# Kernel optimization log

Hardware: AMD Instinct MI355X
Metric: run time of the kernel (lower is better)

The kernel has to match this reference:

```python
import jax, jax.numpy as jnp
import numpy as np


def setup_inputs() -> dict:
    key = jax.random.key(0)
    k1, k2, k3, k4 = jax.random.split(key, 4)
    T = 64            # decoder_batch_len (target steps)
    B = 32            # batch_size
    V = 50257         # decoder vocab size
    L = 400           # encoder (source) length
    rows = T * B
    vocab_ds = jax.random.uniform(k1, (rows, V), dtype=jnp.float32)
    attns = jax.random.uniform(k2, (rows, L), dtype=jnp.float32)
    p_gens = jax.random.uniform(k3, (rows, 1), dtype=jnp.float32)
    sources = jax.random.randint(k4, (L, B), 0, V, dtype=jnp.int64)
    return {
        "vocab_ds": vocab_ds,
        "attns": attns,
        "p_gens": p_gens,
        "sources": sources,
        "decoder_batch_len": T,
    }


def reference(vocab_ds, attns, p_gens, sources, decoder_batch_len):
    # vocab_ds: (T*B, V), attns: (T*B, L), p_gens: (T*B, 1), sources: (L, B)
    rows, V = vocab_ds.shape
    vocab_dists = p_gens * vocab_ds                      # gated generation dist
    attn_dists = (1.0 - p_gens) * attns                  # gated copy dist
    # sources.T tiled over decoder steps -> per-row vocab ids, shape (T*B, L)
    sources_rep = jnp.tile(sources.T, (decoder_batch_len, 1))
    row_idx = jnp.arange(rows)[:, None]                  # (T*B, 1) broadcasts over L
    # torch scatter_ (overwrite semantics) of copy probs into vocab slots
    attn_dists_projected = jnp.zeros((rows, V), dtype=vocab_ds.dtype).at[
        row_idx, sources_rep
    ].set(attn_dists, mode="drop")
    final_dists = attn_dists_projected + vocab_dists
    return final_dists
```

## Files before the change

### kernel.cpp

```cpp
#include <hip/hip_runtime.h>

typedef float f32x4 __attribute__((ext_vector_type(4)));

#define LMAX 1024

__global__ __launch_bounds__(256) void mask_kernel(
    const int* __restrict__ sources, int* __restrict__ vlast, int L, int B)
{
    const int b = blockIdx.x;
    __shared__ int s_col[LMAX];
    const bool use_lds = (L <= LMAX);
    if (use_lds) {
        for (int l = threadIdx.x; l < L; l += blockDim.x)
            s_col[l] = sources[(size_t)l * B + b];
    }
    __syncthreads();
    for (int l = threadIdx.x; l < L; l += blockDim.x) {
        const int v = use_lds ? s_col[l] : sources[(size_t)l * B + b];
        int keep = v;
        if (use_lds) {
            for (int l2 = l + 1; l2 < L; ++l2)
                if (s_col[l2] == v) { keep = -1; break; }
        } else {
            for (int l2 = l + 1; l2 < L; ++l2)
                if (sources[(size_t)l2 * B + b] == v) { keep = -1; break; }
        }
        vlast[(size_t)l * B + b] = keep;
    }
}

__global__ __launch_bounds__(256) void scale_kernel(
    const float* __restrict__ vd, const float* __restrict__ pgs,
    float* __restrict__ out, int V)
{
    const int row = blockIdx.x;
    const int tid = threadIdx.x;
    const size_t base = (size_t)row * (size_t)V;
    const float pg = pgs[row];

    const int mis  = (int)(base & 3);
    const int pre  = mis ? (4 - mis) : 0;
    const int preN = pre < V ? pre : V;
    for (int j = tid; j < preN; j += 256)
        __builtin_nontemporal_store(pg * vd[base + j], &out[base + j]);

    const int nvec = (V - preN) >> 2;
    const f32x4* __restrict__ v4 = (const f32x4*)(vd + base + preN);
    f32x4* __restrict__ o4       = (f32x4*)(out + base + preN);

    int i = tid;
    for (; i + 3 * 256 < nvec; i += 4 * 256) {
        f32x4 a = v4[i];
        f32x4 b = v4[i + 256];
        f32x4 c = v4[i + 512];
        f32x4 d = v4[i + 768];
        a *= pg; b *= pg; c *= pg; d *= pg;
        __builtin_nontemporal_store(a, &o4[i]);
        __builtin_nontemporal_store(b, &o4[i + 256]);
        __builtin_nontemporal_store(c, &o4[i + 512]);
        __builtin_nontemporal_store(d, &o4[i + 768]);
    }
    for (; i < nvec; i += 256) {
        f32x4 a = v4[i];
        a *= pg;
        __builtin_nontemporal_store(a, &o4[i]);
    }
    for (int j = preN + (nvec << 2) + tid; j < V; j += 256)
        __builtin_nontemporal_store(pg * vd[base + j], &out[base + j]);
}

__global__ __launch_bounds__(128) void scatter_kernel(
    const float* __restrict__ vd, const float* __restrict__ attns,
    const float* __restrict__ pgs, const int* __restrict__ vlast,
    float* __restrict__ out, int V, int L, int B)
{
    const int row = blockIdx.x;
    const int b = row % B;
    const float pg = pgs[row];
    const float gate = 1.0f - pg;
    const size_t base = (size_t)row * (size_t)V;
    for (int l = threadIdx.x; l < L; l += 128) {
        const int v = vlast[(size_t)l * B + b];
        if (v >= 0 && v < V)
            out[base + v] = fmaf(pg, vd[base + v],
                                 gate * attns[(size_t)row * L + l]);
    }
}

__global__ __launch_bounds__(256) void fused_fallback_kernel(
    const float* __restrict__ vocab_ds, const float* __restrict__ attns,
    const float* __restrict__ p_gens, const int* __restrict__ sources,
    float* __restrict__ out, int V, int L, int B)
{
    const int row = blockIdx.x;
    const int tid = threadIdx.x;
    const size_t base = (size_t)row * (size_t)V;
    const float pg = p_gens[row];

    const int mis  = (int)(base & 3);
    const int pre  = mis ? (4 - mis) : 0;
    const int preN = pre < V ? pre : V;
    for (int j = tid; j < preN; j += blockDim.x)
        out[base + j] = pg * vocab_ds[base + j];
    const int nvec = (V - preN) >> 2;
    const f32x4* __restrict__ v4 = (const f32x4*)(vocab_ds + base + preN);
    f32x4* __restrict__ o4       = (f32x4*)(out + base + preN);
    for (int i = tid; i < nvec; i += blockDim.x) {
        f32x4 x = v4[i];
        x *= pg;
        o4[i] = x;
    }
    for (int j = preN + (nvec << 2) + tid; j < V; j += blockDim.x)
        out[base + j] = pg * vocab_ds[base + j];

    __shared__ int s_src[512];
    const int b = row % B;
    const bool use_lds = (L <= 512);
    if (use_lds) {
        for (int l = tid; l < L; l += blockDim.x)
            s_src[l] = sources[(size_t)l * B + b];
    }
    __syncthreads();
    const float gate = 1.0f - pg;
    for (int l = tid; l < L; l += blockDim.x) {
        const int v = use_lds ? s_src[l] : sources[(size_t)l * B + b];
        if (v < 0 || v >= V) continue;
        bool last = true;
        for (int l2 = l + 1; l2 < L; ++l2) {
            const int v2 = use_lds ? s_src[l2] : sources[(size_t)l2 * B + b];
            if (v2 == v) { last = false; break; }
        }
        if (last) {
            const float a = gate * attns[(size_t)row * L + l];
            out[base + v] = pg * vocab_ds[base + v] + a;
        }
    }
}

extern "C" void kernel_launch(void* const* d_in, const int* in_sizes, int n_in,
                              void* d_out, int out_size, void* d_ws, size_t ws_size,
                              hipStream_t stream) {
    const float* vocab_ds = (const float*)d_in[0];
    const float* attns    = (const float*)d_in[1];
    const float* p_gens   = (const float*)d_in[2];
    const int*   sources  = (const int*)d_in[3];
    const int rows = in_sizes[2];
    const int V    = in_sizes[0] / rows;
    const int L    = in_sizes[1] / rows;
    const int B    = in_sizes[3] / L;
    float* out = (float*)d_out;

    const size_t mask_bytes = (size_t)L * (size_t)B * sizeof(int);
    if (ws_size >= mask_bytes) {
        int* vlast = (int*)d_ws;
        mask_kernel<<<B, 256, 0, stream>>>(sources, vlast, L, B);
        scale_kernel<<<rows, 256, 0, stream>>>(vocab_ds, p_gens, out, V);
        scatter_kernel<<<rows, 128, 0, stream>>>(vocab_ds, attns, p_gens,
                                                 vlast, out, V, L, B);
    } else {
        fused_fallback_kernel<<<rows, 256, 0, stream>>>(
            vocab_ds, attns, p_gens, sources, out, V, L, B);
    }
}
```

Baseline: 248.6 us.

## Split each row of scale kernel across multiple blocks and use regular stores

The scale kernel now launches several blocks per row, each handling a contiguous chunk of the row's float4 vectors, instead of one block per row. This raises the number of in-flight blocks so memory bandwidth is easier to saturate. Nontemporal stores and the 4-way unrolled loop are replaced by plain stores in a simple loop, so written data may now stay in cache for the scatter kernel to read. The scatter kernel's block size goes from 128 to 256 threads.

```diff
diff --git a/kernel.cpp b/kernel.cpp
--- a/kernel.cpp
+++ b/kernel.cpp
@@ -31,45 +31,39 @@
 
 __global__ __launch_bounds__(256) void scale_kernel(
     const float* __restrict__ vd, const float* __restrict__ pgs,
-    float* __restrict__ out, int V)
+    float* __restrict__ out, int V, int CPR)
 {
-    const int row = blockIdx.x;
-    const int tid = threadIdx.x;
+    const int bid   = blockIdx.x;
+    const int row   = bid / CPR;
+    const int chunk = bid - row * CPR;
+    const int tid   = threadIdx.x;
     const size_t base = (size_t)row * (size_t)V;
     const float pg = pgs[row];
 
     const int mis  = (int)(base & 3);
     const int pre  = mis ? (4 - mis) : 0;
     const int preN = pre < V ? pre : V;
-    for (int j = tid; j < preN; j += 256)
-        __builtin_nontemporal_store(pg * vd[base + j], &out[base + j]);
+    const int nvec = (V - preN) >> 2;
+    const int per  = (nvec + CPR - 1) / CPR;
+    const int v0   = chunk * per;
+    const int v1   = (v0 + per < nvec) ? (v0 + per) : nvec;
 
-    const int nvec = (V - preN) >> 2;
     const f32x4* __restrict__ v4 = (const f32x4*)(vd + base + preN);
     f32x4* __restrict__ o4       = (f32x4*)(out + base + preN);
-
-    int i = tid;
-    for (; i + 3 * 256 < nvec; i += 4 * 256) {
-        f32x4 a = v4[i];
-        f32x4 b = v4[i + 256];
-        f32x4 c = v4[i + 512];
-        f32x4 d = v4[i + 768];
-        a *= pg; b *= pg; c *= pg; d *= pg;
-        __builtin_nontemporal_store(a, &o4[i]);
-        __builtin_nontemporal_store(b, &o4[i + 256]);
-        __builtin_nontemporal_store(c, &o4[i + 512]);
-        __builtin_nontemporal_store(d, &o4[i + 768]);
+    for (int i = v0 + tid; i < v1; i += 256) {
+        f32x4 x = v4[i];
+        x *= pg;
+        o4[i] = x;
     }
-    for (; i < nvec; i += 256) {
-        f32x4 a = v4[i];
-        a *= pg;
-        __builtin_nontemporal_store(a, &o4[i]);
-    }
-    for (int j = preN + (nvec << 2) + tid; j < V; j += 256)
-        __builtin_nontemporal_store(pg * vd[base + j], &out[base + j]);
+    if (chunk == 0)
+        for (int j = tid; j < preN; j += 256)
+            out[base + j] = pg * vd[base + j];
+    if (chunk == CPR - 1)
+        for (int j = preN + (nvec << 2) + tid; j < V; j += 256)
+            out[base + j] = pg * vd[base + j];
 }
 
-__global__ __launch_bounds__(128) void scatter_kernel(
+__global__ __launch_bounds__(256) void scatter_kernel(
     const float* __restrict__ vd, const float* __restrict__ attns,
     const float* __restrict__ pgs, const int* __restrict__ vlast,
     float* __restrict__ out, int V, int L, int B)
@@ -79,7 +73,7 @@
     const float pg = pgs[row];
     const float gate = 1.0f - pg;
     const size_t base = (size_t)row * (size_t)V;
-    for (int l = threadIdx.x; l < L; l += 128) {
+    for (int l = threadIdx.x; l < L; l += 256) {
         const int v = vlast[(size_t)l * B + b];
         if (v >= 0 && v < V)
             out[base + v] = fmaf(pg, vd[base + v],
@@ -153,9 +147,10 @@
     const size_t mask_bytes = (size_t)L * (size_t)B * sizeof(int);
     if (ws_size >= mask_bytes) {
         int* vlast = (int*)d_ws;
+        const int CPR = 8;
         mask_kernel<<<B, 256, 0, stream>>>(sources, vlast, L, B);
-        scale_kernel<<<rows, 256, 0, stream>>>(vocab_ds, p_gens, out, V);
-        scatter_kernel<<<rows, 128, 0, stream>>>(vocab_ds, attns, p_gens,
+        scale_kernel<<<rows * CPR, 256, 0, stream>>>(vocab_ds, p_gens, out, V, CPR);
+        scatter_kernel<<<rows, 256, 0, stream>>>(vocab_ds, attns, p_gens,
                                                  vlast, out, V, L, B);
     } else {
         fused_fallback_kernel<<<rows, 256, 0, stream>>>(
```

Result: slower. 269.8 us (+8.5%).

## Use persistent multi-row scale blocks with LDS occupancy cap and plain stores

Applied to the files above, without the earlier changes.

The scale kernel now launches a fixed grid of 512 blocks, each looping over several rows. A large dummy shared-memory array, referenced only under an impossible condition, limits how many blocks fit per CU. Nontemporal stores are replaced with ordinary stores. The mask kernel switches to a branchless duplicate scan without early exit, and the scatter kernel moves from 128 to 256 threads. The aim is to reduce scheduling overhead and cache contention on the bandwidth-bound pass, at the risk of lower occupancy and less latency hiding.

```diff
diff --git a/kernel.cpp b/kernel.cpp
--- a/kernel.cpp
+++ b/kernel.cpp
@@ -11,65 +11,77 @@
     __shared__ int s_col[LMAX];
     const bool use_lds = (L <= LMAX);
     if (use_lds) {
-        for (int l = threadIdx.x; l < L; l += blockDim.x)
+        for (int l = threadIdx.x; l < L; l += 256)
             s_col[l] = sources[(size_t)l * B + b];
     }
     __syncthreads();
-    for (int l = threadIdx.x; l < L; l += blockDim.x) {
+    for (int l = threadIdx.x; l < L; l += 256) {
         const int v = use_lds ? s_col[l] : sources[(size_t)l * B + b];
-        int keep = v;
+        int dup = 0;
         if (use_lds) {
+#pragma unroll 4
             for (int l2 = l + 1; l2 < L; ++l2)
-                if (s_col[l2] == v) { keep = -1; break; }
+                dup |= (s_col[l2] == v);
         } else {
             for (int l2 = l + 1; l2 < L; ++l2)
-                if (sources[(size_t)l2 * B + b] == v) { keep = -1; break; }
+                dup |= (sources[(size_t)l2 * B + b] == v);
         }
-        vlast[(size_t)l * B + b] = keep;
+        vlast[(size_t)l * B + b] = dup ? -1 : v;
     }
 }
 
+#define SCALE_BLOCKS 512
+
 __global__ __launch_bounds__(256) void scale_kernel(
     const float* __restrict__ vd, const float* __restrict__ pgs,
-    float* __restrict__ out, int V)
+    float* __restrict__ out, int V, int rows, int rpb)
 {
-    const int row = blockIdx.x;
+    __shared__ float lds_cap[16640];
+    if (blockIdx.x > 0x7FFFFFF0u) {
+        lds_cap[threadIdx.x] = pgs[0];
+        out[0] = lds_cap[0];
+    }
     const int tid = threadIdx.x;
-    const size_t base = (size_t)row * (size_t)V;
-    const float pg = pgs[row];
+    const int r0 = blockIdx.x * rpb;
+    const int r1 = (r0 + rpb < rows) ? (r0 + rpb) : rows;
 
-    const int mis  = (int)(base & 3);
-    const int pre  = mis ? (4 - mis) : 0;
-    const int preN = pre < V ? pre : V;
-    for (int j = tid; j < preN; j += 256)
-        __builtin_nontemporal_store(pg * vd[base + j], &out[base + j]);
+    for (int row = r0; row < r1; ++row) {
+        const size_t base = (size_t)row * (size_t)V;
+        const float pg = pgs[row];
 
-    const int nvec = (V - preN) >> 2;
-    const f32x4* __restrict__ v4 = (const f32x4*)(vd + base + preN);
-    f32x4* __restrict__ o4       = (f32x4*)(out + base + preN);
+        const int mis  = (int)(base & 3);
+        const int pre  = mis ? (4 - mis) : 0;
+        const int preN = pre < V ? pre : V;
+        if (tid < preN)
+            out[base + tid] = pg * vd[base + tid];
 
-    int i = tid;
-    for (; i + 3 * 256 < nvec; i += 4 * 256) {
-        f32x4 a = v4[i];
-        f32x4 b = v4[i + 256];
-        f32x4 c = v4[i + 512];
-        f32x4 d = v4[i + 768];
-        a *= pg; b *= pg; c *= pg; d *= pg;
-        __builtin_nontemporal_store(a, &o4[i]);
-        __builtin_nontemporal_store(b, &o4[i + 256]);
-        __builtin_nontemporal_store(c, &o4[i + 512]);
-        __builtin_nontemporal_store(d, &o4[i + 768]);
+        const int nvec = (V - preN) >> 2;
+        const f32x4* __restrict__ v4 = (const f32x4*)(vd + base + preN);
+        f32x4* __restrict__ o4       = (f32x4*)(out + base + preN);
+
+        int i = tid;
+        for (; i + 768 < nvec; i += 1024) {
+            f32x4 a = v4[i];
+            f32x4 b = v4[i + 256];
+            f32x4 c = v4[i + 512];
+            f32x4 d = v4[i + 768];
+            a *= pg; b *= pg; c *= pg; d *= pg;
+            o4[i]       = a;
+            o4[i + 256] = b;
+            o4[i + 512] = c;
+            o4[i + 768] = d;
+        }
+        for (; i < nvec; i += 256) {
+            f32x4 a = v4[i];
+            a *= pg;
+            o4[i] = a;
+        }
+        for (int j = preN + (nvec << 2) + tid; j < V; j += 256)
+            out[base + j] = pg * vd[base + j];
     }
-    for (; i < nvec; i += 256) {
-        f32x4 a = v4[i];
-        a *= pg;
-        __builtin_nontemporal_store(a, &o4[i]);
-    }
-    for (int j = preN + (nvec << 2) + tid; j < V; j += 256)
-        __builtin_nontemporal_store(pg * vd[base + j], &out[base + j]);
 }
 
-__global__ __launch_bounds__(128) void scatter_kernel(
+__global__ __launch_bounds__(256) void scatter_kernel(
     const float* __restrict__ vd, const float* __restrict__ attns,
     const float* __restrict__ pgs, const int* __restrict__ vlast,
     float* __restrict__ out, int V, int L, int B)
@@ -79,7 +91,7 @@
     const float pg = pgs[row];
     const float gate = 1.0f - pg;
     const size_t base = (size_t)row * (size_t)V;
-    for (int l = threadIdx.x; l < L; l += 128) {
+    for (int l = threadIdx.x; l < L; l += 256) {
         const int v = vlast[(size_t)l * B + b];
         if (v >= 0 && v < V)
             out[base + v] = fmaf(pg, vd[base + v],
@@ -153,9 +165,11 @@
     const size_t mask_bytes = (size_t)L * (size_t)B * sizeof(int);
     if (ws_size >= mask_bytes) {
         int* vlast = (int*)d_ws;
+        const int nblk = (rows < SCALE_BLOCKS) ? rows : SCALE_BLOCKS;
+        const int rpb  = (rows + nblk - 1) / nblk;
         mask_kernel<<<B, 256, 0, stream>>>(sources, vlast, L, B);
-        scale_kernel<<<rows, 256, 0, stream>>>(vocab_ds, p_gens, out, V);
-        scatter_kernel<<<rows, 128, 0, stream>>>(vocab_ds, attns, p_gens,
+        scale_kernel<<<nblk, 256, 0, stream>>>(vocab_ds, p_gens, out, V, rows, rpb);
+        scatter_kernel<<<rows, 256, 0, stream>>>(vocab_ds, attns, p_gens,
                                                  vlast, out, V, L, B);
     } else {
         fused_fallback_kernel<<<rows, 256, 0, stream>>>(
```

New measurement: 262.7 us. 1.06x slower.
